# Performance work log

Hardware: AMD Instinct MI355X
Metric: run time of the kernel (lower is better)

Reference implementation:

```python
import jax, jax.numpy as jnp
import numpy as np

N_NODES = 200000
N_EDGES = 3200000
NX = 8
NK = 2


def _l2norm(x, eps=1e-12):
    # F.normalize(x, p=2, dim=-1)
    n = jnp.linalg.norm(x, axis=-1, keepdims=True)
    return x / jnp.maximum(n, eps)


def _aniso_conv(x, src, dst, Kw, n_nodes):
    """For each kernel j: out_j[t] = sum_{e: dst[e]=t} Kw[j,e] * x[src[e]].
    Concatenate over kernels along the feature axis."""
    g = x[src]  # [E, d] gather
    def agg(w):  # w: [E]
        return jax.ops.segment_sum(w[:, None] * g, dst, num_segments=n_nodes)
    out = jax.vmap(agg)(Kw)  # [nk, N, d]
    return jnp.transpose(out, (1, 0, 2)).reshape(n_nodes, -1)  # [N, nk*d]


def setup_inputs() -> dict:
    key = jax.random.key(0)
    ks = jax.random.split(key, 8)
    x = jax.random.normal(ks[0], (N_NODES, NX), dtype=jnp.float32)
    src = jax.random.randint(ks[1], (N_EDGES,), 0, N_NODES, dtype=jnp.int64 if jax.config.jax_enable_x64 else jnp.int32)
    dst = jax.random.randint(ks[2], (N_EDGES,), 0, N_NODES, dtype=src.dtype)
    edge_index = jnp.stack([src, dst], axis=0)
    Kw = jax.random.normal(ks[3], (NK, N_EDGES), dtype=jnp.float32)
    d0, d1 = NX * NK, NX * NK * 2          # 16, 32
    d2 = d1 * NK                            # 64
    hidden, out_ch = 128, 64
    W0 = jax.random.normal(ks[4], (d0, d1), dtype=jnp.float32) / np.sqrt(d0)
    b0 = jnp.zeros((d1,), dtype=jnp.float32)
    W1 = jax.random.normal(ks[5], (d2, hidden), dtype=jnp.float32) / np.sqrt(d2)
    b1 = jnp.zeros((hidden,), dtype=jnp.float32)
    W2 = jax.random.normal(ks[6], (hidden, out_ch), dtype=jnp.float32) / np.sqrt(hidden)
    b2 = jnp.zeros((out_ch,), dtype=jnp.float32)
    return {"x": x, "edge_index": edge_index, "Kw": Kw,
            "W0": W0, "b0": b0, "W1": W1, "b1": b1, "W2": W2, "b2": b2}


def reference(x, edge_index, Kw, W0, b0, W1, b1, W2, b2):
    src, dst = edge_index[0], edge_index[1]
    n = x.shape[0]
    # layer 0: AnisoConv -> single-linear MLP -> L2 normalize
    h = _aniso_conv(x, src, dst, Kw, n)      # [N, 16]
    h = h @ W0 + b0                           # [N, 32]
    h = _l2norm(h)
    # layer 1: AnisoConv -> 2-layer MLP (ReLU between) -> L2 normalize
    h = _aniso_conv(h, src, dst, Kw, n)      # [N, 64]
    h = jax.nn.relu(h @ W1 + b1)             # [N, 128]
    h = h @ W2 + b2                           # [N, 64]
    h = _l2norm(h)
    return h
```

## Files before the change

### kernel.cpp

```cpp
#include <hip/hip_runtime.h>

#define NN 200000
#define NE 3200000
#define NB_SCAN 782
#define NBUCK 391
#define BSHIFT 9
#define BMASK 511
#define SRCMASK 0x3FFFFu
#define NBLK_A 1024
#define EPB (NE / NBLK_A)
#define SSHIFT 15
#define EMAX 18
#define NT_MLP1 12500

using bf16x8 = __attribute__((ext_vector_type(8))) short;
using f32x4  = __attribute__((ext_vector_type(4))) float;

__device__ __forceinline__ float bflo(unsigned u) { return __uint_as_float(u << 16); }
__device__ __forceinline__ float bfhi(unsigned u) { return __uint_as_float(u & 0xffff0000u); }
__device__ __forceinline__ unsigned short f2bfu(float f) {
  unsigned u = __float_as_uint(f);
  return (unsigned short)((u + 0x7fffu + ((u >> 16) & 1u)) >> 16);
}
__device__ __forceinline__ unsigned pack2(float a, float b) {
  return (unsigned)f2bfu(a) | ((unsigned)f2bfu(b) << 16);
}

__device__ __forceinline__ void acc_edge(uint2 e, uint4 u, float* g0, float* g1) {
  float k0 = bflo(e.y), k1 = bfhi(e.y);
  float v0 = bflo(u.x), v1 = bfhi(u.x);
  float v2 = bflo(u.y), v3 = bfhi(u.y);
  float v4 = bflo(u.z), v5 = bfhi(u.z);
  float v6 = bflo(u.w), v7 = bfhi(u.w);
  g0[0] += k0 * v0; g0[1] += k0 * v1; g0[2] += k0 * v2; g0[3] += k0 * v3;
  g0[4] += k0 * v4; g0[5] += k0 * v5; g0[6] += k0 * v6; g0[7] += k0 * v7;
  g1[0] += k1 * v0; g1[1] += k1 * v1; g1[2] += k1 * v2; g1[3] += k1 * v3;
  g1[4] += k1 * v4; g1[5] += k1 * v5; g1[6] += k1 * v6; g1[7] += k1 * v7;
}


__global__ __launch_bounds__(256) void bhist_kernel(const int* __restrict__ dst,
                                                    int* __restrict__ bhT,
                                                    const float* __restrict__ x,
                                                    unsigned short* __restrict__ xbf) {
  __shared__ int h[NBUCK];
  for (int k = threadIdx.x; k < NBUCK; k += 256) h[k] = 0;
  __syncthreads();

  int nid = blockIdx.x * 256 + threadIdx.x;
  if (nid < NN) {
    const float4* xp = reinterpret_cast<const float4*>(x + (size_t)nid * 8);
    float4 a = xp[0], b = xp[1];
    uint4 u;
    u.x = pack2(a.x, a.y); u.y = pack2(a.z, a.w);
    u.z = pack2(b.x, b.y); u.w = pack2(b.z, b.w);
    *reinterpret_cast<uint4*>(xbf + (size_t)nid * 8) = u;
  }

  int base = blockIdx.x * EPB;
  for (int i = threadIdx.x; i < EPB; i += 256)
    atomicAdd(&h[dst[base + i] >> BSHIFT], 1);
  __syncthreads();
  for (int k = threadIdx.x; k < NBUCK; k += 256)
    bhT[k * NBLK_A + blockIdx.x] = h[k];
}

__global__ __launch_bounds__(NBLK_A) void bscan_kernel(const int* __restrict__ bhT,
                                                       int* __restrict__ bhE,
                                                       int* __restrict__ btot) {
  __shared__ int s[NBLK_A];
  int b = blockIdx.x;
  int v = bhT[b * NBLK_A + threadIdx.x];
  s[threadIdx.x] = v;
  __syncthreads();
#pragma unroll
  for (int off = 1; off < NBLK_A; off <<= 1) {
    int t = (threadIdx.x >= off) ? s[threadIdx.x - off] : 0;
    __syncthreads();
    s[threadIdx.x] += t;
    __syncthreads();
  }
  bhE[b * NBLK_A + threadIdx.x] = s[threadIdx.x] - v;
  if (threadIdx.x == NBLK_A - 1) btot[b] = s[NBLK_A - 1];
}

__global__ __launch_bounds__(512) void bbase_kernel(const int* __restrict__ btot,
                                                    int* __restrict__ bbase) {
  __shared__ int s[512];
  int v = (threadIdx.x < NBUCK) ? btot[threadIdx.x] : 0;
  s[threadIdx.x] = v;
  __syncthreads();
#pragma unroll
  for (int off = 1; off < 512; off <<= 1) {
    int t = (threadIdx.x >= off) ? s[threadIdx.x - off] : 0;
    __syncthreads();
    s[threadIdx.x] += t;
    __syncthreads();
  }
  if (threadIdx.x < NBUCK) bbase[threadIdx.x] = s[threadIdx.x] - v;
  if (threadIdx.x == NBUCK - 1) bbase[NBUCK] = s[threadIdx.x];
}

__global__ __launch_bounds__(512) void bplace_kernel(
    const int* __restrict__ src, const int* __restrict__ dst,
    const float* __restrict__ kw, const int* __restrict__ bhT,
    const int* __restrict__ bhE, const int* __restrict__ bbase,
    uint2* __restrict__ bsorted) {
  __shared__ uint2 stage[EPB];
  __shared__ unsigned short stageK[EPB];
  __shared__ int sc[512];
  __shared__ int hv[512];
  __shared__ int gof[512];
  __shared__ int cur[512];
  int tid = threadIdx.x, blk = blockIdx.x;
  int base = blk * EPB;

  int v = (tid < NBUCK) ? bhT[tid * NBLK_A + blk] : 0;
  hv[tid] = v;
  sc[tid] = v;
  __syncthreads();
#pragma unroll
  for (int off = 1; off < 512; off <<= 1) {
    int t = (tid >= off) ? sc[tid - off] : 0;
    __syncthreads();
    sc[tid] += t;
    __syncthreads();
  }
  int excl = sc[tid] - hv[tid];
  cur[tid] = excl;
  if (tid < NBUCK)
    gof[tid] = bbase[tid] + bhE[tid * NBLK_A + blk] - excl;
  __syncthreads();
  for (int i = tid; i < EPB; i += 512) {
    int e = base + i;
    int d = dst[e];
    int k = d >> BSHIFT;
    int p = atomicAdd(&cur[k], 1);
    uint2 u;
    u.x = (unsigned)src[e] | ((unsigned)(d & BMASK) << 18);
    u.y = pack2(kw[e], kw[NE + e]);
    stage[p] = u;
    stageK[p] = (unsigned short)k;
  }
  __syncthreads();
  for (int i = tid; i < EPB; i += 512) {
    int k = stageK[i];
    bsorted[gof[k] + i] = stage[i];
  }
}


__global__ __launch_bounds__(512) void nsort_kernel(
    const uint2* __restrict__ bsorted, const int* __restrict__ bbase,
    int* __restrict__ cnt, int* __restrict__ offs, uint2* __restrict__ sedge) {
  __shared__ int h4[4096];
  __shared__ int cur4[4096];
  __shared__ int s[512];
  int tid = threadIdx.x, b = blockIdx.x;
  for (int j = tid; j < 4096; j += 512) h4[j] = 0;
  __syncthreads();
  int r0 = bbase[b], r1 = bbase[b + 1];
  int i0 = r0 + tid;

  uint2 e[EMAX];
#pragma unroll
  for (int j = 0; j < EMAX; ++j) {
    int i = i0 + j * 512;
    if (i < r1) {
      e[j] = bsorted[i];
      int key = (int)((e[j].x >> 18) << 3) | (int)((e[j].x & SRCMASK) >> SSHIFT);
      atomicAdd(&h4[key], 1);
    }
  }
  for (int i = i0 + EMAX * 512; i < r1; i += 512) {
    unsigned ex = bsorted[i].x;
    int key = (int)((ex >> 18) << 3) | (int)((ex & SRCMASK) >> SSHIFT);
    atomicAdd(&h4[key], 1);
  }
  __syncthreads();

  int loc[8];
  int sum = 0;
#pragma unroll
  for (int k = 0; k < 8; ++k) {
    loc[k] = sum;
    sum += h4[tid * 8 + k];
  }
  s[tid] = sum;
  __syncthreads();
#pragma unroll
  for (int off = 1; off < 512; off <<= 1) {
    int t = (tid >= off) ? s[tid - off] : 0;
    __syncthreads();
    s[tid] += t;
    __syncthreads();
  }
  int nbase = r0 + s[tid] - sum;
  int node = b * 512 + tid;
  if (node < NN) { cnt[node] = sum; offs[node] = nbase; }
#pragma unroll
  for (int k = 0; k < 8; ++k) cur4[tid * 8 + k] = nbase + loc[k];
  __syncthreads();

#pragma unroll
  for (int j = 0; j < EMAX; ++j) {
    int i = i0 + j * 512;
    if (i < r1) {
      int key = (int)((e[j].x >> 18) << 3) | (int)((e[j].x & SRCMASK) >> SSHIFT);
      int pos = atomicAdd(&cur4[key], 1);
      uint2 w; w.x = e[j].x & SRCMASK; w.y = e[j].y;
      sedge[pos] = w;
    }
  }
  for (int i = i0 + EMAX * 512; i < r1; i += 512) {
    uint2 u = bsorted[i];
    int key = (int)((u.x >> 18) << 3) | (int)((u.x & SRCMASK) >> SSHIFT);
    int pos = atomicAdd(&cur4[key], 1);
    u.x &= SRCMASK;
    sedge[pos] = u;
  }
}


__global__ __launch_bounds__(256) void fused0_kernel(
    const unsigned short* __restrict__ xbf, const int* __restrict__ offs,
    const int* __restrict__ cnt, const uint2* __restrict__ sedge,
    const float* __restrict__ W0, const float* __restrict__ b0,
    unsigned short* __restrict__ h1bf) {
  __shared__ float w0t[32][16];
  __shared__ float b0s[32];
  int tid = threadIdx.x;
  for (int i = tid; i < 16 * 32; i += 256) {
    int k = i >> 5, j = i & 31;
    w0t[j][k] = W0[i];
  }
  if (tid < 32) b0s[tid] = b0[tid];
  __syncthreads();

  int node = blockIdx.x * 256 + tid;
  if (node >= NN) return;

  int start = offs[node];
  int deg = cnt[node];
  float ha[8], hb[8];
#pragma unroll
  for (int k = 0; k < 8; ++k) { ha[k] = 0.f; hb[k] = 0.f; }

  int i = 0;
  for (; i + 4 <= deg; i += 4) {
    uint2 ee[4];
    uint4 uu[4];
#pragma unroll
    for (int j = 0; j < 4; ++j) ee[j] = sedge[start + i + j];
#pragma unroll
    for (int j = 0; j < 4; ++j)
      uu[j] = *reinterpret_cast<const uint4*>(xbf + (size_t)ee[j].x * 8);
#pragma unroll
    for (int j = 0; j < 4; ++j) acc_edge(ee[j], uu[j], ha, hb);
  }
  for (; i < deg; ++i) {
    uint2 e = sedge[start + i];
    uint4 u = *reinterpret_cast<const uint4*>(xbf + (size_t)e.x * 8);
    acc_edge(e, u, ha, hb);
  }

  float o[32];
  float ss = 0.f;
#pragma unroll
  for (int j = 0; j < 32; ++j) {
    float acc = b0s[j];
#pragma unroll
    for (int k = 0; k < 8; ++k) acc += ha[k] * w0t[j][k];
#pragma unroll
    for (int k = 0; k < 8; ++k) acc += hb[k] * w0t[j][8 + k];
    o[j] = acc;
    ss += acc * acc;
  }
  float inv = 1.f / fmaxf(sqrtf(ss), 1e-12f);
  uint4* op = reinterpret_cast<uint4*>(h1bf + (size_t)node * 32);
#pragma unroll
  for (int c = 0; c < 4; ++c) {
    uint4 u;
    u.x = pack2(o[c * 8 + 0] * inv, o[c * 8 + 1] * inv);
    u.y = pack2(o[c * 8 + 2] * inv, o[c * 8 + 3] * inv);
    u.z = pack2(o[c * 8 + 4] * inv, o[c * 8 + 5] * inv);
    u.w = pack2(o[c * 8 + 6] * inv, o[c * 8 + 7] * inv);
    op[c] = u;
  }
}


__global__ __launch_bounds__(256) void gather1_kernel(
    const unsigned short* __restrict__ h1bf, const int* __restrict__ offs,
    const int* __restrict__ cnt, const uint2* __restrict__ sedge,
    unsigned short* __restrict__ gbf) {
  int idx = blockIdx.x * 256 + threadIdx.x;
  int node = idx >> 2, q = idx & 3;
  int start = offs[node];
  int deg = cnt[node];

  float g0[8], g1[8];
#pragma unroll
  for (int k = 0; k < 8; ++k) { g0[k] = 0.f; g1[k] = 0.f; }

  int i = 0;
  for (; i + 8 <= deg; i += 8) {
    uint2 ee[8];
    uint4 uu[8];
#pragma unroll
    for (int j = 0; j < 8; ++j) ee[j] = sedge[start + i + j];
#pragma unroll
    for (int j = 0; j < 8; ++j)
      uu[j] = *reinterpret_cast<const uint4*>(h1bf + (size_t)ee[j].x * 32 + q * 8);
#pragma unroll
    for (int j = 0; j < 8; ++j) acc_edge(ee[j], uu[j], g0, g1);
  }
  for (; i + 4 <= deg; i += 4) {
    uint2 ee[4];
    uint4 uu[4];
#pragma unroll
    for (int j = 0; j < 4; ++j) ee[j] = sedge[start + i + j];
#pragma unroll
    for (int j = 0; j < 4; ++j)
      uu[j] = *reinterpret_cast<const uint4*>(h1bf + (size_t)ee[j].x * 32 + q * 8);
#pragma unroll
    for (int j = 0; j < 4; ++j) acc_edge(ee[j], uu[j], g0, g1);
  }
  for (; i < deg; ++i) {
    uint2 e = sedge[start + i];
    uint4 u = *reinterpret_cast<const uint4*>(h1bf + (size_t)e.x * 32 + q * 8);
    acc_edge(e, u, g0, g1);
  }

  uint4 s0, s1;
  s0.x = pack2(g0[0], g0[1]); s0.y = pack2(g0[2], g0[3]);
  s0.z = pack2(g0[4], g0[5]); s0.w = pack2(g0[6], g0[7]);
  s1.x = pack2(g1[0], g1[1]); s1.y = pack2(g1[2], g1[3]);
  s1.z = pack2(g1[4], g1[5]); s1.w = pack2(g1[6], g1[7]);
  *reinterpret_cast<uint4*>(gbf + (size_t)node * 64 + q * 8) = s0;
  *reinterpret_cast<uint4*>(gbf + (size_t)node * 64 + 32 + q * 8) = s1;
}


__global__ __launch_bounds__(256) void mlp1_kernel(
    const unsigned short* __restrict__ gbf,
    const float* __restrict__ W1, const float* __restrict__ b1,
    const float* __restrict__ W2, const float* __restrict__ b2,
    float* __restrict__ out) {
  __shared__ __align__(16) short hlds[4][16][136];
  int tid = threadIdx.x;
  int wave = tid >> 6, lane = tid & 63;
  int lg = lane >> 4;
  int lr = lane & 15;

  bf16x8 w1f[8][2];
#pragma unroll
  for (int n = 0; n < 8; ++n)
#pragma unroll
    for (int ks = 0; ks < 2; ++ks) {
      bf16x8 f;
#pragma unroll
      for (int i = 0; i < 8; ++i)
        f[i] = (short)f2bfu(W1[(size_t)(ks * 32 + lg * 8 + i) * 128 + n * 16 + lr]);
      w1f[n][ks] = f;
    }
  bf16x8 w2f[4][4];
#pragma unroll
  for (int n2 = 0; n2 < 4; ++n2)
#pragma unroll
    for (int ks = 0; ks < 4; ++ks) {
      bf16x8 f;
#pragma unroll
      for (int i = 0; i < 8; ++i)
        f[i] = (short)f2bfu(W2[(size_t)(ks * 32 + lg * 8 + i) * 64 + n2 * 16 + lr]);
      w2f[n2][ks] = f;
    }
  float b1v[8], b2v[4];
#pragma unroll
  for (int n = 0; n < 8; ++n) b1v[n] = b1[n * 16 + lr];
#pragma unroll
  for (int n2 = 0; n2 < 4; ++n2) b2v[n2] = b2[n2 * 16 + lr];

  for (int tile = blockIdx.x * 4 + wave; tile < NT_MLP1; tile += gridDim.x * 4) {
    int base = tile * 16;
    const bf16x8* grow = reinterpret_cast<const bf16x8*>(gbf + (size_t)(base + lr) * 64);
    bf16x8 a1_0 = grow[lg];
    bf16x8 a1_1 = grow[4 + lg];

#pragma unroll
    for (int n = 0; n < 8; ++n) {
      f32x4 acc = {0.f, 0.f, 0.f, 0.f};
      acc = __builtin_amdgcn_mfma_f32_16x16x32_bf16(a1_0, w1f[n][0], acc, 0, 0, 0);
      acc = __builtin_amdgcn_mfma_f32_16x16x32_bf16(a1_1, w1f[n][1], acc, 0, 0, 0);
#pragma unroll
      for (int q = 0; q < 4; ++q) {
        float v = fmaxf(acc[q] + b1v[n], 0.f);
        hlds[wave][lg * 4 + q][n * 16 + lr] = (short)f2bfu(v);
      }
    }

    bf16x8 a2[4];
#pragma unroll
    for (int ks = 0; ks < 4; ++ks)
      a2[ks] = *reinterpret_cast<const bf16x8*>(&hlds[wave][lr][ks * 32 + lg * 8]);
    f32x4 acc2[4];
#pragma unroll
    for (int n2 = 0; n2 < 4; ++n2) {
      f32x4 a = {0.f, 0.f, 0.f, 0.f};
#pragma unroll
      for (int ks = 0; ks < 4; ++ks)
        a = __builtin_amdgcn_mfma_f32_16x16x32_bf16(a2[ks], w2f[n2][ks], a, 0, 0, 0);
      acc2[n2] = a;
    }

#pragma unroll
    for (int q = 0; q < 4; ++q) {
      float s = 0.f;
#pragma unroll
      for (int n2 = 0; n2 < 4; ++n2) {
        float v = acc2[n2][q] + b2v[n2];
        s += v * v;
      }
      s += __shfl_xor(s, 1); s += __shfl_xor(s, 2);
      s += __shfl_xor(s, 4); s += __shfl_xor(s, 8);
      float inv = 1.f / fmaxf(sqrtf(s), 1e-12f);
      size_t rowoff = (size_t)(base + lg * 4 + q) * 64 + lr;
#pragma unroll
      for (int n2 = 0; n2 < 4; ++n2)
        out[rowoff + n2 * 16] = (acc2[n2][q] + b2v[n2]) * inv;
    }
  }
}


extern "C" void kernel_launch(void* const* d_in, const int* in_sizes, int n_in,
                              void* d_out, int out_size, void* d_ws, size_t ws_size,
                              hipStream_t stream) {
  const float* x  = (const float*)d_in[0];
  const int* ei   = (const int*)d_in[1];
  const float* kw = (const float*)d_in[2];
  const float* W0 = (const float*)d_in[3];
  const float* b0 = (const float*)d_in[4];
  const float* W1 = (const float*)d_in[5];
  const float* b1 = (const float*)d_in[6];
  const float* W2 = (const float*)d_in[7];
  const float* b2 = (const float*)d_in[8];
  float* out = (float*)d_out;

  const int* src = ei;
  const int* dst = ei + NE;

  char* p = (char*)d_ws;
  uint2* bsorted = (uint2*)p;                p += (size_t)NE * 8;
  uint2* sedge   = (uint2*)p;                p += (size_t)NE * 8;
  unsigned short* h1bf = (unsigned short*)p; p += (size_t)NN * 32 * 2;
  unsigned short* xbf  = (unsigned short*)p; p += (size_t)NN * 8 * 2;
  int* bhT   = (int*)p;                      p += (size_t)NBUCK * NBLK_A * 4;
  int* bhE   = (int*)p;                      p += (size_t)NBUCK * NBLK_A * 4;
  int* btot  = (int*)p;                      p += (size_t)NBUCK * 4;
  int* bbase = (int*)p;                      p += (size_t)(NBUCK + 1) * 4;
  int* cnt   = (int*)p;                      p += (size_t)NN * 4;
  int* offs  = (int*)p;                      p += (size_t)NN * 4;
  unsigned short* gbf = (unsigned short*)bsorted;

  bhist_kernel<<<NBLK_A, 256, 0, stream>>>(dst, bhT, x, xbf);
  bscan_kernel<<<NBUCK, NBLK_A, 0, stream>>>(bhT, bhE, btot);
  bbase_kernel<<<1, 512, 0, stream>>>(btot, bbase);
  bplace_kernel<<<NBLK_A, 512, 0, stream>>>(src, dst, kw, bhT, bhE, bbase, bsorted);

  nsort_kernel<<<NBUCK, 512, 0, stream>>>(bsorted, bbase, cnt, offs, sedge);

  fused0_kernel<<<NB_SCAN, 256, 0, stream>>>(xbf, offs, cnt, sedge, W0, b0, h1bf);
  gather1_kernel<<<(4 * NN) / 256, 256, 0, stream>>>(h1bf, offs, cnt, sedge, gbf);
  mlp1_kernel<<<768, 256, 0, stream>>>(gbf, W1, b1, W2, b2, out);
}
```

Before: 203.1 us.

## Fuse node sort with layer-0 aggregation and MLP into one kernel

Merges the per-bucket node sort kernel with the layer-0 gather/aggregate/linear/normalize kernel. After sorting a 512-node bucket into shared-memory-derived offsets, each thread processes its own node directly, using its locally computed base and degree. This drops one launch and the re-reading of offsets and counts, and may hit the freshly written sorted edges in cache. In exchange, the layer-0 work now runs at 391 blocks of 512 threads instead of 782 of 256, and the sort kernel's shared memory grows slightly.

```diff
diff --git a/kernel.cpp b/kernel.cpp
--- a/kernel.cpp
+++ b/kernel.cpp
@@ -2,7 +2,6 @@
 
 #define NN 200000
 #define NE 3200000
-#define NB_SCAN 782
 #define NBUCK 391
 #define BSHIFT 9
 #define BMASK 511
@@ -150,14 +149,26 @@
 }
 
 
-__global__ __launch_bounds__(512) void nsort_kernel(
+__global__ __launch_bounds__(512) void nsf_kernel(
     const uint2* __restrict__ bsorted, const int* __restrict__ bbase,
-    int* __restrict__ cnt, int* __restrict__ offs, uint2* __restrict__ sedge) {
+    int* __restrict__ cnt, int* __restrict__ offs, uint2* __restrict__ sedge,
+    const unsigned short* __restrict__ xbf,
+    const float* __restrict__ W0, const float* __restrict__ b0,
+    unsigned short* __restrict__ h1bf) {
   __shared__ int h4[4096];
   __shared__ int cur4[4096];
   __shared__ int s[512];
+  __shared__ float w0t[32][16];
+  __shared__ float b0s[32];
   int tid = threadIdx.x, b = blockIdx.x;
   for (int j = tid; j < 4096; j += 512) h4[j] = 0;
+  if (tid < 512) {
+    if (tid < 32) b0s[tid] = b0[tid];
+  }
+  for (int i = tid; i < 16 * 32; i += 512) {
+    int k = i >> 5, j = i & 31;
+    w0t[j][k] = W0[i];
+  }
   __syncthreads();
   int r0 = bbase[b], r1 = bbase[b + 1];
   int i0 = r0 + tid;
@@ -219,29 +230,29 @@
     u.x &= SRCMASK;
     sedge[pos] = u;
   }
-}
-
-
-__global__ __launch_bounds__(256) void fused0_kernel(
-    const unsigned short* __restrict__ xbf, const int* __restrict__ offs,
-    const int* __restrict__ cnt, const uint2* __restrict__ sedge,
-    const float* __restrict__ W0, const float* __restrict__ b0,
-    unsigned short* __restrict__ h1bf) {
-  __shared__ float w0t[32][16];
-  __shared__ float b0s[32];
-  int tid = threadIdx.x;
-  for (int i = tid; i < 16 * 32; i += 256) {
-    int k = i >> 5, j = i & 31;
-    w0t[j][k] = W0[i];
-  }
-  if (tid < 32) b0s[tid] = b0[tid];
-  __syncthreads();
-
-  int node = blockIdx.x * 256 + tid;
-  if (node >= NN) return;
-
-  int start = offs[node];
-  int deg = cnt[node];
+  __syncthreads();
+
+  if (node >= NN || sum == 0) {
+    if (node < NN) {
+      float o[32]; float ss = 0.f;
+#pragma unroll
+      for (int j = 0; j < 32; ++j) { o[j] = b0s[j]; ss += o[j] * o[j]; }
+      float inv = 1.f / fmaxf(sqrtf(ss), 1e-12f);
+      uint4* op = reinterpret_cast<uint4*>(h1bf + (size_t)node * 32);
+#pragma unroll
+      for (int c = 0; c < 4; ++c) {
+        uint4 u;
+        u.x = pack2(o[c * 8 + 0] * inv, o[c * 8 + 1] * inv);
+        u.y = pack2(o[c * 8 + 2] * inv, o[c * 8 + 3] * inv);
+        u.z = pack2(o[c * 8 + 4] * inv, o[c * 8 + 5] * inv);
+        u.w = pack2(o[c * 8 + 6] * inv, o[c * 8 + 7] * inv);
+        op[c] = u;
+      }
+    }
+    return;
+  }
+
+  int start = nbase, deg = sum;
   float ha[8], hb[8];
 #pragma unroll
   for (int k = 0; k < 8; ++k) { ha[k] = 0.f; hb[k] = 0.f; }
@@ -259,9 +270,9 @@
     for (int j = 0; j < 4; ++j) acc_edge(ee[j], uu[j], ha, hb);
   }
   for (; i < deg; ++i) {
-    uint2 e = sedge[start + i];
-    uint4 u = *reinterpret_cast<const uint4*>(xbf + (size_t)e.x * 8);
-    acc_edge(e, u, ha, hb);
+    uint2 ed = sedge[start + i];
+    uint4 u = *reinterpret_cast<const uint4*>(xbf + (size_t)ed.x * 8);
+    acc_edge(ed, u, ha, hb);
   }
 
   float o[32];
@@ -468,9 +479,9 @@
   bbase_kernel<<<1, 512, 0, stream>>>(btot, bbase);
   bplace_kernel<<<NBLK_A, 512, 0, stream>>>(src, dst, kw, bhT, bhE, bbase, bsorted);
 
-  nsort_kernel<<<NBUCK, 512, 0, stream>>>(bsorted, bbase, cnt, offs, sedge);
-
-  fused0_kernel<<<NB_SCAN, 256, 0, stream>>>(xbf, offs, cnt, sedge, W0, b0, h1bf);
+  nsf_kernel<<<NBUCK, 512, 0, stream>>>(bsorted, bbase, cnt, offs, sedge,
+                                        xbf, W0, b0, h1bf);
+
   gather1_kernel<<<(4 * NN) / 256, 256, 0, stream>>>(h1bf, offs, cnt, sedge, gbf);
   mlp1_kernel<<<768, 256, 0, stream>>>(gbf, W1, b1, W2, b2, out);
 }
```

After: 206.2 us, median of 2. No clear change (+1.5%).
